# Optimization experiments

Measured on AMD Instinct MI355X. Metric: run time of the kernel, lower is better.

The kernel has to match this reference:

```python
import jax, jax.numpy as jnp
import numpy as np

TAU = 1.0
PAD_IDX = 0
EOS_IDX = 3
NEG = -10000000.0

B, T, H, E, V, BN = 256, 256, 1024, 512, 32000, 512


def setup_inputs() -> dict:
    key = jax.random.key(0)
    ks = jax.random.split(key, 30)
    s = lambda *sh: 0.02
    inp = {}
    inp['input_ids'] = jax.random.randint(ks[0], (B,), 0, V)
    inp['prediction'] = jax.random.normal(ks[1], (B, V), jnp.float32)
    inp['context'] = jax.random.normal(ks[2], (B, T, 2 * H), jnp.float32)
    inp['h0'] = jax.random.normal(ks[3], (2, B, H), jnp.float32)
    inp['mask'] = jax.random.randint(ks[4], (B, 8), 0, V)
    # parameters
    inp['embedding'] = jax.random.normal(ks[5], (V, E), jnp.float32) * 0.02
    inp['ge1_w'] = jax.random.normal(ks[6], (E, E), jnp.float32) * 0.02
    inp['ge1_b'] = jnp.zeros((E,), jnp.float32)
    inp['ge2_w'] = jax.random.normal(ks[7], (E, E), jnp.float32) * 0.02
    inp['ge2_b'] = jnp.zeros((E,), jnp.float32)
    inp['att_we'] = jax.random.normal(ks[8], (2 * H, H), jnp.float32) * 0.02
    inp['att_wd'] = jax.random.normal(ks[9], (H, H), jnp.float32) * 0.02
    inp['att_v'] = jax.random.normal(ks[10], (H,), jnp.float32) * 0.02
    in0 = 2 * H + E
    inp['wih0'] = jax.random.normal(ks[11], (3 * H, in0), jnp.float32) * 0.02
    inp['whh0'] = jax.random.normal(ks[12], (3 * H, H), jnp.float32) * 0.02
    inp['bih0'] = jnp.zeros((3 * H,), jnp.float32)
    inp['bhh0'] = jnp.zeros((3 * H,), jnp.float32)
    inp['wih1'] = jax.random.normal(ks[13], (3 * H, H), jnp.float32) * 0.02
    inp['whh1'] = jax.random.normal(ks[14], (3 * H, H), jnp.float32) * 0.02
    inp['bih1'] = jnp.zeros((3 * H,), jnp.float32)
    inp['bhh1'] = jnp.zeros((3 * H,), jnp.float32)
    inp['bn0_w'] = jax.random.normal(ks[15], (3 * H + E, BN), jnp.float32) * 0.02
    inp['bn0_b'] = jnp.zeros((BN,), jnp.float32)
    inp['bn1_w'] = jax.random.normal(ks[16], (BN, V), jnp.float32) * 0.02
    inp['bn1_b'] = jnp.zeros((V,), jnp.float32)
    return inp


def _gru_cell(x, h, wih, whh, bih, bhh):
    gi = x @ wih.T + bih  # [B, 3H]
    gh = h @ whh.T + bhh
    gi_r, gi_z, gi_n = jnp.split(gi, 3, axis=1)
    gh_r, gh_z, gh_n = jnp.split(gh, 3, axis=1)
    r = jax.nn.sigmoid(gi_r + gh_r)
    z = jax.nn.sigmoid(gi_z + gh_z)
    n = jnp.tanh(gi_n + r * gh_n)
    return (1.0 - z) * n + z * h


def _forward(input_ids, prediction, context, h0, mask, embedding,
             ge1_w, ge1_b, ge2_w, ge2_b, att_we, att_wd, att_v,
             wih0, whh0, bih0, bhh0, wih1, whh1, bih1, bhh1,
             bn0_w, bn0_b, bn1_w, bn1_b):
    embs = embedding[input_ids]  # [B, E]
    # global embedding gate
    probs = jax.nn.softmax(prediction / TAU, axis=1)  # [B, V]
    emb_avg = probs @ embedding  # [B, E]
    Hg = jax.nn.sigmoid(embs @ ge1_w + ge1_b + emb_avg @ ge2_w + ge2_b)
    embs = Hg * embs + (1.0 - Hg) * emb_avg
    # bahdanau attention with query = top-layer hidden
    q = h0[-1]  # [B, H]
    scores = jnp.tanh(context @ att_we + (q @ att_wd)[:, None, :]) @ att_v  # [B, T]
    attn = jax.nn.softmax(scores, axis=1)
    c_t = jnp.einsum('bt,btd->bd', attn, context)  # [B, 2H]
    rnn_in = jnp.concatenate([embs, c_t], axis=1)  # [B, E+2H]
    h1_0 = _gru_cell(rnn_in, h0[0], wih0, whh0, bih0, bhh0)
    h1_1 = _gru_cell(h1_0, h0[1], wih1, whh1, bih1, bhh1)
    output = h1_1
    h1 = jnp.stack([h1_0, h1_1])
    b0 = jnp.tanh(jnp.concatenate([output, c_t, embs], axis=1) @ bn0_w + bn0_b)
    pred = b0 @ bn1_w + bn1_b  # [B, V]
    # masked scatter: forbid already-generated tokens, but keep PAD/EOS columns
    pad_col = pred[:, PAD_IDX]
    eos_col = pred[:, EOS_IDX]
    rows = jnp.arange(pred.shape[0])
    pred = pred.at[rows[:, None], mask].set(NEG)
    pred = pred.at[:, PAD_IDX].set(pad_col)
    pred = pred.at[:, EOS_IDX].set(eos_col)
    return pred, h1, attn


def reference(input_ids, prediction, context, h0, mask, embedding,
              ge1_w, ge1_b, ge2_w, ge2_b, att_we, att_wd, att_v,
              wih0, whh0, bih0, bhh0, wih1, whh1, bih1, bhh1,
              bn0_w, bn0_b, bn1_w, bn1_b):
    return _forward(input_ids, prediction, context, h0, mask, embedding,
                    ge1_w, ge1_b, ge2_w, ge2_b, att_we, att_wd, att_v,
                    wih0, whh0, bih0, bhh0, wih1, whh1, bih1, bhh1,
                    bn0_w, bn0_b, bn1_w, bn1_b)
```

## Files before the change

### kernel.cpp

```cpp
#include <hip/hip_runtime.h>
#include <hip/hip_bf16.h>


typedef unsigned short u16;
typedef unsigned int u32;
typedef float f32x4 __attribute__((ext_vector_type(4)));
typedef u32 u32x4 __attribute__((ext_vector_type(4)));
typedef __bf16 bf16x8 __attribute__((ext_vector_type(8)));
typedef short s16x8 __attribute__((ext_vector_type(8)));

__device__ __forceinline__ u16 f2bf(float x) {
  u32 u = __float_as_uint(x);
  u += 0x7fffu + ((u >> 16) & 1u);
  return (u16)(u >> 16);
}
__device__ __forceinline__ u32 pack2(float a, float b) {
  return (u32)f2bf(a) | ((u32)f2bf(b) << 16);
}
__device__ __forceinline__ u32 cvt2(float a, float b) {
  union { __bf16 h[2]; u32 w; } u;
  u.h[0] = (__bf16)a; u.h[1] = (__bf16)b;
  return u.w;
}
__device__ __forceinline__ float bf2f(u16 v) {
  return __uint_as_float((u32)v << 16);
}
__device__ __forceinline__ f32x4 mfma_bf16(s16x8 a, s16x8 b, f32x4 c) {
  union { s16x8 s; bf16x8 b; } ua, ub;
  ua.s = a; ub.s = b;
  return __builtin_amdgcn_mfma_f32_16x16x32_bf16(ua.b, ub.b, c, 0, 0, 0);
}
__device__ __forceinline__ void gll16(const void* g, void* l) {
  __builtin_amdgcn_global_load_lds((__attribute__((address_space(1))) void*)g,
                                   (__attribute__((address_space(3))) void*)l,
                                   16, 0, 0);
}
__device__ __forceinline__ float sigf(float x) { return 1.0f / (1.0f + __expf(-x)); }

__global__ __launch_bounds__(256) void k_cvt8(const float* __restrict__ s,
                                              u16* __restrict__ d)
{
  size_t i = ((size_t)blockIdx.x * 256 + threadIdx.x) * 8;
  const size_t stride = (size_t)gridDim.x * 2048;
  for (; i < 134217728ull; i += stride) {
    float4 a = *(const float4*)(s + i);
    float4 b = *(const float4*)(s + i + 4);
    u32x4 w = {cvt2(a.x, a.y), cvt2(a.z, a.w), cvt2(b.x, b.y), cvt2(b.z, b.w)};
    *(u32x4*)(d + i) = w;
  }
}

__global__ __launch_bounds__(512, 4) void k_scores_bf(
    const u16* __restrict__ A, const u16* __restrict__ weT,
    const float* __restrict__ qd, const float* __restrict__ att_v,
    float* __restrict__ scores)
{
  __shared__ u16 As[3][4096];
  __shared__ u16 Bs[3][8192];

  const int tid = threadIdx.x;
  const int lane = tid & 63, wid = tid >> 6;
  const int l15 = lane & 15, lg = lane >> 4;
  const int wm = wid >> 2, wn = wid & 3;

  const int f = blockIdx.x;
  const int xcd = f & 7, slot = f >> 3;
  const int ntile = slot & 3;
  const int mtile = (slot >> 2) * 8 + xcd;
  const int n0 = ntile * 256;
  const int m0 = mtile * 128;
  const int b = mtile >> 1;

  const int sslot = ((lane & 3) ^ ((lane >> 3) & 3)) * 8;
  const size_t asrc = (size_t)(m0 + wid * 16 + (lane >> 2)) * 2048 + sslot;
  size_t bsrc[2];
#pragma unroll
  for (int i = 0; i < 2; ++i)
    bsrc[i] = (size_t)(n0 + (wid * 2 + i) * 16 + (lane >> 2)) * 2048 + sslot;

  const int rslot = (lg ^ ((l15 >> 1) & 3)) * 8;
  int aoff[4], boff[4];
#pragma unroll
  for (int mf = 0; mf < 4; ++mf) aoff[mf] = (wm * 64 + mf * 16 + l15) * 32 + rslot;
#pragma unroll
  for (int nf = 0; nf < 4; ++nf) boff[nf] = (wn * 64 + nf * 16 + l15) * 32 + rslot;

  f32x4 acc[4][4];
#pragma unroll
  for (int mf = 0; mf < 4; ++mf)
#pragma unroll
    for (int nf = 0; nf < 4; ++nf) acc[mf][nf] = (f32x4){0.f, 0.f, 0.f, 0.f};

  u16* As0 = &As[0][0];
  u16* Bs0 = &Bs[0][0];

  {
    gll16(A + asrc, As0 + wid * 512);
#pragma unroll
    for (int i = 0; i < 2; ++i)
      gll16(weT + bsrc[i], Bs0 + (wid * 2 + i) * 512);
    gll16(A + asrc + 32, As0 + 4096 + wid * 512);
#pragma unroll
    for (int i = 0; i < 2; ++i)
      gll16(weT + bsrc[i] + 32, Bs0 + 8192 + (wid * 2 + i) * 512);
  }

  int cur = 0, stg = 2;
  for (int kt = 0; kt < 64; ++kt) {
    if (kt < 63) asm volatile("s_waitcnt vmcnt(3)" ::: "memory");
    else         asm volatile("s_waitcnt vmcnt(0)" ::: "memory");
    __builtin_amdgcn_s_barrier();
    __builtin_amdgcn_sched_barrier(0);
    if (kt + 2 < 64) {
      gll16(A + asrc + (size_t)(kt + 2) * 32, As0 + stg * 4096 + wid * 512);
#pragma unroll
      for (int i = 0; i < 2; ++i)
        gll16(weT + bsrc[i] + (size_t)(kt + 2) * 32,
              Bs0 + stg * 8192 + (wid * 2 + i) * 512);
    }
    s16x8 af[4], bf[4];
#pragma unroll
    for (int mf = 0; mf < 4; ++mf)
      af[mf] = *(const s16x8*)(As0 + cur * 4096 + aoff[mf]);
#pragma unroll
    for (int nf = 0; nf < 4; ++nf)
      bf[nf] = *(const s16x8*)(Bs0 + cur * 8192 + boff[nf]);
    __builtin_amdgcn_s_setprio(1);
#pragma unroll
    for (int nf = 0; nf < 4; ++nf)
#pragma unroll
      for (int mf = 0; mf < 4; ++mf)
        acc[mf][nf] = mfma_bf16(af[mf], bf[nf], acc[mf][nf]);
    __builtin_amdgcn_s_setprio(0);
    cur = (cur == 2) ? 0 : cur + 1;
    stg = (stg == 2) ? 0 : stg + 1;
  }

  float rp[4][4] = {{0.f, 0.f, 0.f, 0.f}, {0.f, 0.f, 0.f, 0.f},
                    {0.f, 0.f, 0.f, 0.f}, {0.f, 0.f, 0.f, 0.f}};
#pragma unroll
  for (int nf = 0; nf < 4; ++nf) {
    int col = n0 + wn * 64 + nf * 16 + l15;
    float qv = qd[(size_t)b * 1024 + col];
    float vv = att_v[col];
#pragma unroll
    for (int mf = 0; mf < 4; ++mf)
#pragma unroll
      for (int e = 0; e < 4; ++e)
        rp[mf][e] += tanhf(acc[mf][nf][e] + qv) * vv;
  }
#pragma unroll
  for (int d = 1; d < 16; d <<= 1)
#pragma unroll
    for (int mf = 0; mf < 4; ++mf)
#pragma unroll
      for (int e = 0; e < 4; ++e)
        rp[mf][e] += __shfl_xor(rp[mf][e], d);
  if (l15 == 0) {
#pragma unroll
    for (int mf = 0; mf < 4; ++mf)
#pragma unroll
      for (int e = 0; e < 4; ++e)
        atomicAdd(&scores[(size_t)m0 + wm * 64 + mf * 16 + lg * 4 + e], rp[mf][e]);
  }
}

__global__ __launch_bounds__(256, 3) void k_scores(
    const float* __restrict__ ctx, const u16* __restrict__ weT,
    const float* __restrict__ qd, const float* __restrict__ att_v,
    float* __restrict__ scores)
{
  __shared__ u16 As[2][4096];
  __shared__ u16 Bs[2][4096];

  const int tid = threadIdx.x;
  const int lane = tid & 63, wid = tid >> 6;
  const int l15 = lane & 15, lg = lane >> 4;
  const int wm = wid >> 1, wn = wid & 1;
  const int n0 = blockIdx.x * 128;
  const int m0 = blockIdx.y * 128;
  const int b = blockIdx.y >> 1;

  const int r0 = tid >> 3, c4 = tid & 7;
  const float* actx = ctx + (size_t)(m0 + r0) * 2048 + c4 * 4;
  const int awoff = r0 * 32 + c4 * 4;

  size_t bsrc[2];
#pragma unroll
  for (int i = 0; i < 2; ++i)
    bsrc[i] = (size_t)(n0 + (wid * 2 + i) * 16 + (lane >> 2)) * 2048 + (size_t)(lane & 3) * 8;

  int aoff[4], boff[4];
#pragma unroll
  for (int mf = 0; mf < 4; ++mf) aoff[mf] = (wm * 64 + mf * 16 + l15) * 32 + lg * 8;
#pragma unroll
  for (int nf = 0; nf < 4; ++nf) boff[nf] = (wn * 64 + nf * 16 + l15) * 32 + lg * 8;

  f32x4 acc[4][4];
#pragma unroll
  for (int mf = 0; mf < 4; ++mf)
#pragma unroll
    for (int nf = 0; nf < 4; ++nf) acc[mf][nf] = (f32x4){0.f, 0.f, 0.f, 0.f};

  {
#pragma unroll
    for (int i = 0; i < 2; ++i)
      gll16(weT + bsrc[i], &Bs[0][(wid * 2 + i) * 512]);
#pragma unroll
    for (int j = 0; j < 4; ++j) {
      float4 av = *(const float4*)(actx + (size_t)(j * 32) * 2048);
      u32* w = (u32*)&As[0][awoff + j * 1024];
      w[0] = cvt2(av.x, av.y); w[1] = cvt2(av.z, av.w);
    }
  }
  __syncthreads();

  for (int kt = 0; kt < 64; ++kt) {
    const int cur = kt & 1, nxt = cur ^ 1;
    const bool pf = (kt < 63);
    float4 av[4];
    if (pf) {
#pragma unroll
      for (int i = 0; i < 2; ++i)
        gll16(weT + bsrc[i] + (size_t)(kt + 1) * 32, &Bs[nxt][(wid * 2 + i) * 512]);
#pragma unroll
      for (int j = 0; j < 4; ++j)
        av[j] = *(const float4*)(actx + (size_t)(j * 32) * 2048 + (kt + 1) * 32);
    }
    s16x8 af[4], bf[4];
#pragma unroll
    for (int mf = 0; mf < 4; ++mf) af[mf] = *(const s16x8*)(&As[cur][0] + aoff[mf]);
#pragma unroll
    for (int nf = 0; nf < 4; ++nf) bf[nf] = *(const s16x8*)(&Bs[cur][0] + boff[nf]);
#pragma unroll
    for (int nf = 0; nf < 4; ++nf)
#pragma unroll
      for (int mf = 0; mf < 4; ++mf)
        acc[mf][nf] = mfma_bf16(af[mf], bf[nf], acc[mf][nf]);
    if (pf) {
#pragma unroll
      for (int j = 0; j < 4; ++j) {
        u32* w = (u32*)&As[nxt][awoff + j * 1024];
        w[0] = cvt2(av[j].x, av[j].y); w[1] = cvt2(av[j].z, av[j].w);
      }
    }
    __syncthreads();
  }

  float rp[4][4] = {{0.f, 0.f, 0.f, 0.f}, {0.f, 0.f, 0.f, 0.f},
                    {0.f, 0.f, 0.f, 0.f}, {0.f, 0.f, 0.f, 0.f}};
#pragma unroll
  for (int nf = 0; nf < 4; ++nf) {
    int col = n0 + wn * 64 + nf * 16 + l15;
    float qv = qd[(size_t)b * 1024 + col];
    float vv = att_v[col];
#pragma unroll
    for (int mf = 0; mf < 4; ++mf)
#pragma unroll
      for (int e = 0; e < 4; ++e)
        rp[mf][e] += tanhf(acc[mf][nf][e] + qv) * vv;
  }
#pragma unroll
  for (int d = 1; d < 16; d <<= 1)
#pragma unroll
    for (int mf = 0; mf < 4; ++mf)
#pragma unroll
      for (int e = 0; e < 4; ++e)
        rp[mf][e] += __shfl_xor(rp[mf][e], d);
  if (l15 == 0) {
#pragma unroll
    for (int mf = 0; mf < 4; ++mf)
#pragma unroll
      for (int e = 0; e < 4; ++e)
        atomicAdd(&scores[(size_t)m0 + wm * 64 + mf * 16 + lg * 4 + e], rp[mf][e]);
  }
}

template <int MODE>
__global__ __launch_bounds__(256, 2) void k_gemm(
    const u16* __restrict__ A, const float* __restrict__ W,
    float* __restrict__ C, const float* __restrict__ bias,
    int N, int K, int ksteps_per, int tot_ksteps, int atomic_mode)
{
  __shared__ u16 As[2][8192];
  __shared__ u16 Bs[2][2048];
  const int tid = threadIdx.x, lane = tid & 63, wid = tid >> 6;
  const int l15 = lane & 15, lg = lane >> 4;
  const int m0 = blockIdx.x * 256;
  const int n0 = blockIdx.y * 64;
  const int kc0 = blockIdx.z * ksteps_per;
  int kcn = tot_ksteps - kc0;
  if (kcn > ksteps_per) kcn = ksteps_per;

  size_t asrc[4];
#pragma unroll
  for (int j = 0; j < 4; ++j)
    asrc[j] = (size_t)(m0 + wid * 64 + j * 16 + (lane >> 2)) * K + (size_t)(lane & 3) * 8;
  int aoff[4], boff[4];
#pragma unroll
  for (int mf = 0; mf < 4; ++mf) aoff[mf] = (wid * 64 + mf * 16 + l15) * 32 + lg * 8;
#pragma unroll
  for (int nf = 0; nf < 4; ++nf) boff[nf] = (nf * 16 + l15) * 32 + lg * 8;

  const int b_row = tid >> 2, b_c8 = tid & 3;
  const int b_kk = tid >> 3, b_c4 = tid & 7;

  f32x4 acc[4][4];
#pragma unroll
  for (int mf = 0; mf < 4; ++mf)
#pragma unroll
    for (int nf = 0; nf < 4; ++nf) acc[mf][nf] = (f32x4){0.f, 0.f, 0.f, 0.f};

  {
#pragma unroll
    for (int j = 0; j < 4; ++j)
      gll16(A + asrc[j] + (size_t)kc0 * 32, &As[0][wid * 2048 + j * 512]);
    if (MODE == 0) {
      const float* p = W + (size_t)(n0 + b_row) * K + (size_t)kc0 * 32 + b_c8 * 8;
      float4 v0 = *(const float4*)p, v1 = *(const float4*)(p + 4);
      u32* w = (u32*)&Bs[0][b_row * 32 + b_c8 * 8];
      w[0] = pack2(v0.x, v0.y); w[1] = pack2(v0.z, v0.w);
      w[2] = pack2(v1.x, v1.y); w[3] = pack2(v1.z, v1.w);
    } else {
      const float* p = W + (size_t)(kc0 * 32 + b_kk) * N + n0 + b_c4 * 4;
      float4 v0 = *(const float4*)p;
      float4 v1 = *(const float4*)(p + 32);
      int r0 = b_c4 * 4, r1 = 32 + b_c4 * 4;
      Bs[0][(r0 + 0) * 32 + b_kk] = f2bf(v0.x);
      Bs[0][(r0 + 1) * 32 + b_kk] = f2bf(v0.y);
      Bs[0][(r0 + 2) * 32 + b_kk] = f2bf(v0.z);
      Bs[0][(r0 + 3) * 32 + b_kk] = f2bf(v0.w);
      Bs[0][(r1 + 0) * 32 + b_kk] = f2bf(v1.x);
      Bs[0][(r1 + 1) * 32 + b_kk] = f2bf(v1.y);
      Bs[0][(r1 + 2) * 32 + b_kk] = f2bf(v1.z);
      Bs[0][(r1 + 3) * 32 + b_kk] = f2bf(v1.w);
    }
  }
  __syncthreads();

  for (int s = 0; s < kcn; ++s) {
    const int cur = s & 1, nxt = cur ^ 1;
    const bool pf = (s + 1 < kcn);
    const int ktn = kc0 + s + 1;
    float4 v0, v1;
    if (pf) {
#pragma unroll
      for (int j = 0; j < 4; ++j)
        gll16(A + asrc[j] + (size_t)ktn * 32, &As[nxt][wid * 2048 + j * 512]);
      if (MODE == 0) {
        const float* p = W + (size_t)(n0 + b_row) * K + (size_t)ktn * 32 + b_c8 * 8;
        v0 = *(const float4*)p; v1 = *(const float4*)(p + 4);
      } else {
        const float* p = W + (size_t)(ktn * 32 + b_kk) * N + n0 + b_c4 * 4;
        v0 = *(const float4*)p;
        v1 = *(const float4*)(p + 32);
      }
    }
    s16x8 af[4], bf[4];
#pragma unroll
    for (int mf = 0; mf < 4; ++mf) af[mf] = *(const s16x8*)(&As[cur][0] + aoff[mf]);
#pragma unroll
    for (int nf = 0; nf < 4; ++nf) bf[nf] = *(const s16x8*)(&Bs[cur][0] + boff[nf]);
#pragma unroll
    for (int nf = 0; nf < 4; ++nf)
#pragma unroll
      for (int mf = 0; mf < 4; ++mf)
        acc[mf][nf] = mfma_bf16(af[mf], bf[nf], acc[mf][nf]);
    if (pf) {
      if (MODE == 0) {
        u32* w = (u32*)&Bs[nxt][b_row * 32 + b_c8 * 8];
        w[0] = pack2(v0.x, v0.y); w[1] = pack2(v0.z, v0.w);
        w[2] = pack2(v1.x, v1.y); w[3] = pack2(v1.z, v1.w);
      } else {
        int r0 = b_c4 * 4, r1 = 32 + b_c4 * 4;
        Bs[nxt][(r0 + 0) * 32 + b_kk] = f2bf(v0.x);
        Bs[nxt][(r0 + 1) * 32 + b_kk] = f2bf(v0.y);
        Bs[nxt][(r0 + 2) * 32 + b_kk] = f2bf(v0.z);
        Bs[nxt][(r0 + 3) * 32 + b_kk] = f2bf(v0.w);
        Bs[nxt][(r1 + 0) * 32 + b_kk] = f2bf(v1.x);
        Bs[nxt][(r1 + 1) * 32 + b_kk] = f2bf(v1.y);
        Bs[nxt][(r1 + 2) * 32 + b_kk] = f2bf(v1.z);
        Bs[nxt][(r1 + 3) * 32 + b_kk] = f2bf(v1.w);
      }
    }
    __syncthreads();
  }

  const size_t Ns = (size_t)N;
#pragma unroll
  for (int mf = 0; mf < 4; ++mf)
#pragma unroll
    for (int nf = 0; nf < 4; ++nf) {
      int col = n0 + nf * 16 + l15;
#pragma unroll
      for (int e = 0; e < 4; ++e) {
        int row = m0 + wid * 64 + mf * 16 + lg * 4 + e;
        float v = acc[mf][nf][e];
        if (atomic_mode) atomicAdd(&C[row * Ns + col], v);
        else C[row * Ns + col] = v + (bias ? bias[col] : 0.0f);
      }
    }
}

__global__ __launch_bounds__(256) void k_prep(
    const float* __restrict__ we, u16* __restrict__ weT,
    const float* __restrict__ h0, u16* __restrict__ h0_bf,
    const int* __restrict__ ids, const float* __restrict__ emb,
    float* __restrict__ e0, u16* __restrict__ e0b)
{
  __shared__ float t[32][33];
  const int bid = blockIdx.x, tid = threadIdx.x;
  if (bid < 2048) {
    const int n0 = (bid & 31) * 32, k0 = (bid >> 5) * 32;
#pragma unroll
    for (int p = 0; p < 4; ++p) {
      int e = tid + p * 256, r = e >> 5, c = e & 31;
      t[r][c] = we[(size_t)(k0 + r) * 1024 + n0 + c];
    }
    __syncthreads();
#pragma unroll
    for (int p = 0; p < 4; ++p) {
      int e = tid + p * 256, n = e >> 5, k = e & 31;
      weT[(size_t)(n0 + n) * 2048 + k0 + k] = f2bf(t[k][n]);
    }
  } else if (bid < 4096) {
    int i = (bid - 2048) * 256 + tid;
    h0_bf[i] = f2bf(h0[i]);
  } else {
    int b = bid - 4096;
    int id = ids[b];
    for (int i = tid; i < 512; i += 256) {
      float v = emb[(size_t)id * 512 + i];
      e0[(size_t)b * 512 + i] = v;
      e0b[(size_t)b * 512 + i] = f2bf(v);
    }
  }
}

__global__ void k_cast(const float* __restrict__ s, u16* __restrict__ d, int n)
{
  int i = blockIdx.x * 256 + threadIdx.x;
  if (i < n) d[i] = f2bf(s[i]);
}

__global__ __launch_bounds__(1024) void k_softmax_pred(const float* __restrict__ pred,
                                                       u16* __restrict__ probs)
{
  __shared__ u16 xrow[32000];
  __shared__ float smM[16], smS[16];
  const int row = blockIdx.x, tid = threadIdx.x;
  const float* x = pred + (size_t)row * 32000;
  float m = -3.0e38f, s = 0.f;
  for (int i = tid; i < 32000; i += 1024) {
    u16 bv = f2bf(x[i]);
    xrow[i] = bv;
    float vr = bf2f(bv);
    if (vr > m) { s = s * __expf(m - vr) + 1.0f; m = vr; }
    else s += __expf(vr - m);
  }
#pragma unroll
  for (int d = 1; d < 64; d <<= 1) {
    float mo = __shfl_xor(m, d), so = __shfl_xor(s, d);
    float M = fmaxf(m, mo);
    s = s * __expf(m - M) + so * __expf(mo - M);
    m = M;
  }
  if ((tid & 63) == 0) { smM[tid >> 6] = m; smS[tid >> 6] = s; }
  __syncthreads();
  float M = -3.0e38f;
#pragma unroll
  for (int w = 0; w < 16; ++w) M = fmaxf(M, smM[w]);
  float S = 0.f;
#pragma unroll
  for (int w = 0; w < 16; ++w) S += smS[w] * __expf(smM[w] - M);
  float inv = 1.0f / S;
  for (int i = tid; i < 32000; i += 1024)
    probs[(size_t)row * 32000 + i] = f2bf(__expf(bf2f(xrow[i]) - M) * inv);
}

__global__ __launch_bounds__(256) void k_softmax_sc(const float* __restrict__ sc,
                                                    float* __restrict__ attn)
{
  __shared__ float sm[4];
  const int row = blockIdx.x, tid = threadIdx.x;
  float x = sc[(size_t)row * 256 + tid];
  float mx = x;
#pragma unroll
  for (int d = 1; d < 64; d <<= 1) mx = fmaxf(mx, __shfl_xor(mx, d));
  if ((tid & 63) == 0) sm[tid >> 6] = mx;
  __syncthreads();
  mx = fmaxf(fmaxf(sm[0], sm[1]), fmaxf(sm[2], sm[3]));
  float e = __expf(x - mx);
  float s = e;
#pragma unroll
  for (int d = 1; d < 64; d <<= 1) s += __shfl_xor(s, d);
  __syncthreads();
  if ((tid & 63) == 0) sm[tid >> 6] = s;
  __syncthreads();
  s = sm[0] + sm[1] + sm[2] + sm[3];
  attn[(size_t)row * 256 + tid] = e / s;
}

__global__ __launch_bounds__(256) void k_attn_ct(
    const float* __restrict__ sc, const u16* __restrict__ ctxb,
    float* __restrict__ attn, float* __restrict__ c_t)
{
  __shared__ float sm[4];
  __shared__ float att[256];
  const int b = blockIdx.y, tid = threadIdx.x;
  float x = sc[(size_t)b * 256 + tid];
  float mx = x;
#pragma unroll
  for (int d = 1; d < 64; d <<= 1) mx = fmaxf(mx, __shfl_xor(mx, d));
  if ((tid & 63) == 0) sm[tid >> 6] = mx;
  __syncthreads();
  mx = fmaxf(fmaxf(sm[0], sm[1]), fmaxf(sm[2], sm[3]));
  float e = __expf(x - mx);
  float s = e;
#pragma unroll
  for (int d = 1; d < 64; d <<= 1) s += __shfl_xor(s, d);
  __syncthreads();
  if ((tid & 63) == 0) sm[tid >> 6] = s;
  __syncthreads();
  s = sm[0] + sm[1] + sm[2] + sm[3];
  float a = e / s;
  att[tid] = a;
  if (blockIdx.x == 0) attn[(size_t)b * 256 + tid] = a;
  __syncthreads();

  const int d0 = blockIdx.x * 512 + tid * 2;
  const u16* cp = ctxb + (size_t)b * 524288 + d0;
  float a0 = 0.f, a1 = 0.f;
#pragma unroll 8
  for (int t = 0; t < 256; ++t) {
    float av = att[t];
    ushort2 v = *(const ushort2*)(cp + (size_t)t * 2048);
    a0 += av * bf2f(v.x); a1 += av * bf2f(v.y);
  }
  float2* o = (float2*)(c_t + (size_t)b * 2048 + d0);
  *o = (float2){a0, a1};
}

__global__ __launch_bounds__(256) void k_ct(const float* __restrict__ ctx,
                                            const float* __restrict__ attn,
                                            float* __restrict__ c_t)
{
  const int b = blockIdx.y;
  const int d0 = blockIdx.x * 512 + threadIdx.x * 2;
  const float2* cp = (const float2*)(ctx + (size_t)b * 524288 + d0);
  const float* ar = attn + (size_t)b * 256;
  float ax = 0.f, ay = 0.f;
#pragma unroll 4
  for (int t = 0; t < 256; ++t) {
    float a = ar[t];
    float2 v = cp[(size_t)t * 1024];
    ax += a * v.x; ay += a * v.y;
  }
  c_t[(size_t)b * 2048 + d0] = ax;
  c_t[(size_t)b * 2048 + d0 + 1] = ay;
}

__global__ void k_gate_cat(const float* __restrict__ gepre, const float* __restrict__ b1,
                           const float* __restrict__ b2, const float* __restrict__ e0,
                           const float* __restrict__ ea, float* __restrict__ embs,
                           const float* __restrict__ ct, u16* __restrict__ out)
{
  int i = blockIdx.x * 256 + threadIdx.x;
  int m = i / 2560, c = i - m * 2560;
  float v;
  if (c < 512) {
    int idx = m * 512 + c;
    float hg = sigf(gepre[idx] + b1[c] + b2[c]);
    v = hg * e0[idx] + (1.0f - hg) * ea[idx];
    embs[idx] = v;
  } else {
    v = ct[(size_t)m * 2048 + (c - 512)];
  }
  out[i] = f2bf(v);
}

__global__ void k_gru(const float* __restrict__ gi, const float* __restrict__ gh,
                      const float* __restrict__ bih, const float* __restrict__ bhh,
                      const float* __restrict__ hprev, float* __restrict__ hout,
                      u16* __restrict__ hout_bf)
{
  int i = blockIdx.x * 256 + threadIdx.x;
  int m = i >> 10, h = i & 1023;
  const float* gim = gi + (size_t)m * 3072;
  const float* ghm = gh + (size_t)m * 3072;
  float r = sigf(gim[h] + bih[h] + ghm[h] + bhh[h]);
  float z = sigf(gim[1024 + h] + bih[1024 + h] + ghm[1024 + h] + bhh[1024 + h]);
  float n = tanhf(gim[2048 + h] + bih[2048 + h] + r * (ghm[2048 + h] + bhh[2048 + h]));
  float hv = (1.0f - z) * n + z * hprev[i];
  hout[i] = hv;
  if (hout_bf) hout_bf[i] = f2bf(hv);
}

__global__ void k_cat_bn0(const float* __restrict__ h11, const float* __restrict__ ct,
                          const float* __restrict__ embs, u16* __restrict__ out)
{
  int i = blockIdx.x * 256 + threadIdx.x;
  int m = i / 3584, c = i - m * 3584;
  float v;
  if (c < 1024) v = h11[(size_t)m * 1024 + c];
  else if (c < 3072) v = ct[(size_t)m * 2048 + (c - 1024)];
  else v = embs[(size_t)m * 512 + (c - 3072)];
  out[i] = f2bf(v);
}

__global__ void k_bn0(const float* __restrict__ pre, const float* __restrict__ bias,
                      u16* __restrict__ b0b)
{
  int i = blockIdx.x * 256 + threadIdx.x;
  int nn = i & 511;
  b0b[i] = f2bf(tanhf(pre[i] + bias[nn]));
}

__global__ void k_mask(const int* __restrict__ mask, float* __restrict__ pred)
{
  int t = blockIdx.x * 256 + threadIdx.x;
  if (t >= 2048) return;
  int b = t >> 3;
  int col = mask[t];
  if (col != 0 && col != 3) pred[(size_t)b * 32000 + col] = -10000000.0f;
}

extern "C" void kernel_launch(void* const* d_in, const int* in_sizes, int n_in,
                              void* d_out, int out_size, void* d_ws, size_t ws_size,
                              hipStream_t stream)
{
  const int*   input_ids = (const int*)d_in[0];
  const float* prediction= (const float*)d_in[1];
  const float* context   = (const float*)d_in[2];
  const float* h0        = (const float*)d_in[3];
  const int*   maskp     = (const int*)d_in[4];
  const float* embedding = (const float*)d_in[5];
  const float* ge1_w = (const float*)d_in[6];
  const float* ge1_b = (const float*)d_in[7];
  const float* ge2_w = (const float*)d_in[8];
  const float* ge2_b = (const float*)d_in[9];
  const float* att_we = (const float*)d_in[10];
  const float* att_wd = (const float*)d_in[11];
  const float* att_v  = (const float*)d_in[12];
  const float* wih0 = (const float*)d_in[13];
  const float* whh0 = (const float*)d_in[14];
  const float* bih0 = (const float*)d_in[15];
  const float* bhh0 = (const float*)d_in[16];
  const float* wih1 = (const float*)d_in[17];
  const float* whh1 = (const float*)d_in[18];
  const float* bih1 = (const float*)d_in[19];
  const float* bhh1 = (const float*)d_in[20];
  const float* bn0_w = (const float*)d_in[21];
  const float* bn0_b = (const float*)d_in[22];
  const float* bn1_w = (const float*)d_in[23];
  const float* bn1_b = (const float*)d_in[24];

  float* out = (float*)d_out;
  float* out_pred = out;
  float* out_h1_0 = out + 8192000;
  float* out_h1_1 = out + 8454144;
  float* out_attn = out + 8716288;

  char* ws = (char*)d_ws;
  float* qd      = (float*)(ws + 0);
  float* emb_avg = (float*)(ws + 1048576);
  float* gepre   = (float*)(ws + 1572864);
  float* gi0     = (float*)(ws + 2097152);
  float* gh0     = (float*)(ws + 5242880);
  float* gi1     = (float*)(ws + 8388608);
  float* gh1     = (float*)(ws + 11534336);
  float* bn0pre  = (float*)(ws + 14680064);
  float* scores  = (float*)(ws + 15204352);
  const size_t MS_BYTES = 15466496;
  float* c_t     = (float*)(ws + 15466496);
  float* embs0   = (float*)(ws + 17563648);
  float* embs    = (float*)(ws + 18087936);
  u16* weT       = (u16*)(ws + 18612224);
  u16* h0_bf     = (u16*)(ws + 22806528);
  u16* embs0_bf  = (u16*)(ws + 23855104);
  u16* probs_bf  = (u16*)(ws + 24117248);
  u16* embavg_bf = (u16*)(ws + 40501248);
  u16* rnnin_bf  = (u16*)(ws + 40763392);
  u16* h1_0_bf   = (u16*)(ws + 42074112);
  u16* bn0in_bf  = (u16*)(ws + 42598400);
  u16* b0_bf     = (u16*)(ws + 44433408);
  u16* ctx_bf    = (u16*)(ws + 44695552);
  const bool big = ws_size >= 44695552ull + 268435456ull;

  (void)in_sizes; (void)n_in; (void)out_size;

  hipMemsetAsync(ws, 0, MS_BYTES, stream);

  if (big) k_cvt8<<<8192, 256, 0, stream>>>(context, ctx_bf);
  k_prep<<<4352, 256, 0, stream>>>(att_we, weT, h0, h0_bf, input_ids, embedding,
                                   embs0, embs0_bf);
  k_softmax_pred<<<256, 1024, 0, stream>>>(prediction, probs_bf);

  k_gemm<1><<<dim3(1, 16, 8), 256, 0, stream>>>(h0_bf + 262144, att_wd, qd, nullptr,
                                                1024, 1024, 4, 32, 1);
  if (big)
    k_scores_bf<<<2048, 512, 0, stream>>>(ctx_bf, weT, qd, att_v, scores);
  else
    k_scores<<<dim3(8, 512), 256, 0, stream>>>(context, weT, qd, att_v, scores);

  k_gemm<1><<<dim3(1, 8, 50), 256, 0, stream>>>(probs_bf, embedding, emb_avg, nullptr,
                                                512, 32000, 20, 1000, 1);
  k_cast<<<512, 256, 0, stream>>>(emb_avg, embavg_bf, 131072);
  k_gemm<1><<<dim3(1, 8, 4), 256, 0, stream>>>(embs0_bf, ge1_w, gepre, nullptr,
                                               512, 512, 4, 16, 1);
  k_gemm<1><<<dim3(1, 8, 4), 256, 0, stream>>>(embavg_bf, ge2_w, gepre, nullptr,
                                               512, 512, 4, 16, 1);

  if (big) {
    k_attn_ct<<<dim3(4, 256), 256, 0, stream>>>(scores, ctx_bf, out_attn, c_t);
  } else {
    k_softmax_sc<<<256, 256, 0, stream>>>(scores, out_attn);
    k_ct<<<dim3(4, 256), 256, 0, stream>>>(context, out_attn, c_t);
  }

  k_gate_cat<<<2560, 256, 0, stream>>>(gepre, ge1_b, ge2_b, embs0, emb_avg,
                                       embs, c_t, rnnin_bf);

  k_gemm<0><<<dim3(1, 48, 5), 256, 0, stream>>>(rnnin_bf, wih0, gi0, nullptr,
                                                3072, 2560, 16, 80, 1);
  k_gemm<0><<<dim3(1, 48, 4), 256, 0, stream>>>(h0_bf, whh0, gh0, nullptr,
                                                3072, 1024, 8, 32, 1);
  k_gru<<<1024, 256, 0, stream>>>(gi0, gh0, bih0, bhh0, h0, out_h1_0, h1_0_bf);
  k_gemm<0><<<dim3(1, 48, 4), 256, 0, stream>>>(h1_0_bf, wih1, gi1, nullptr,
                                                3072, 1024, 8, 32, 1);
  k_gemm<0><<<dim3(1, 48, 4), 256, 0, stream>>>(h0_bf + 262144, whh1, gh1, nullptr,
                                                3072, 1024, 8, 32, 1);
  k_gru<<<1024, 256, 0, stream>>>(gi1, gh1, bih1, bhh1, h0 + 262144, out_h1_1, nullptr);

  k_cat_bn0<<<3584, 256, 0, stream>>>(out_h1_1, c_t, embs, bn0in_bf);
  k_gemm<1><<<dim3(1, 8, 16), 256, 0, stream>>>(bn0in_bf, bn0_w, bn0pre, nullptr,
                                                512, 3584, 7, 112, 1);
  k_bn0<<<512, 256, 0, stream>>>(bn0pre, bn0_b, b0_bf);
  k_gemm<1><<<dim3(1, 500, 1), 256, 0, stream>>>(b0_bf, bn1_w, out_pred, bn1_b,
                                                 32000, 512, 16, 16, 0);
  k_mask<<<8, 256, 0, stream>>>(maskp, out_pred);
}
```

Before: 802.2 us.

## Drop bf16 context pre-conversion; convert fp32 context inline in scores GEMM

Removes the separate pass that converted the 512 MB fp32 context to bf16. The scores kernel now loads fp32 context directly and converts it to bf16 while staging into LDS, with a double buffer in place of the triple-buffered async load pipeline. The fused softmax and context kernel now reads fp32 context directly. This drops a full read and write of the context tensor. In exchange the scores main loop does register-staged loads and conversion with a barrier every iteration, and the c_t reduction reads twice as many bytes.

```diff
diff --git a/kernel.cpp b/kernel.cpp
--- a/kernel.cpp
+++ b/kernel.cpp
@@ -37,26 +37,13 @@
 }
 __device__ __forceinline__ float sigf(float x) { return 1.0f / (1.0f + __expf(-x)); }
 
-__global__ __launch_bounds__(256) void k_cvt8(const float* __restrict__ s,
-                                              u16* __restrict__ d)
-{
-  size_t i = ((size_t)blockIdx.x * 256 + threadIdx.x) * 8;
-  const size_t stride = (size_t)gridDim.x * 2048;
-  for (; i < 134217728ull; i += stride) {
-    float4 a = *(const float4*)(s + i);
-    float4 b = *(const float4*)(s + i + 4);
-    u32x4 w = {cvt2(a.x, a.y), cvt2(a.z, a.w), cvt2(b.x, b.y), cvt2(b.z, b.w)};
-    *(u32x4*)(d + i) = w;
-  }
-}
-
-__global__ __launch_bounds__(512, 4) void k_scores_bf(
-    const u16* __restrict__ A, const u16* __restrict__ weT,
+__global__ __launch_bounds__(512, 4) void k_scores_f32(
+    const float* __restrict__ ctx, const u16* __restrict__ weT,
     const float* __restrict__ qd, const float* __restrict__ att_v,
     float* __restrict__ scores)
 {
-  __shared__ u16 As[3][4096];
-  __shared__ u16 Bs[3][8192];
+  __shared__ u16 As[2][4096];
+  __shared__ u16 Bs[2][8192];
 
   const int tid = threadIdx.x;
   const int lane = tid & 63, wid = tid >> 6;
@@ -71,8 +58,11 @@
   const int m0 = mtile * 128;
   const int b = mtile >> 1;
 
+  const int arow = tid >> 2, ac8 = (tid & 3) * 8;
+  const float* actx = ctx + (size_t)(m0 + arow) * 2048 + ac8;
+  const int awoff = arow * 32 + ac8;
+
   const int sslot = ((lane & 3) ^ ((lane >> 3) & 3)) * 8;
-  const size_t asrc = (size_t)(m0 + wid * 16 + (lane >> 2)) * 2048 + sslot;
   size_t bsrc[2];
 #pragma unroll
   for (int i = 0; i < 2; ++i)
@@ -81,7 +71,7 @@
   const int rslot = (lg ^ ((l15 >> 1) & 3)) * 8;
   int aoff[4], boff[4];
 #pragma unroll
-  for (int mf = 0; mf < 4; ++mf) aoff[mf] = (wm * 64 + mf * 16 + l15) * 32 + rslot;
+  for (int mf = 0; mf < 4; ++mf) aoff[mf] = (wm * 64 + mf * 16 + l15) * 32 + lg * 8;
 #pragma unroll
   for (int nf = 0; nf < 4; ++nf) boff[nf] = (wn * 64 + nf * 16 + l15) * 32 + rslot;
 
@@ -91,40 +81,33 @@
 #pragma unroll
     for (int nf = 0; nf < 4; ++nf) acc[mf][nf] = (f32x4){0.f, 0.f, 0.f, 0.f};
 
-  u16* As0 = &As[0][0];
-  u16* Bs0 = &Bs[0][0];
-
   {
-    gll16(A + asrc, As0 + wid * 512);
 #pragma unroll
     for (int i = 0; i < 2; ++i)
-      gll16(weT + bsrc[i], Bs0 + (wid * 2 + i) * 512);
-    gll16(A + asrc + 32, As0 + 4096 + wid * 512);
-#pragma unroll
-    for (int i = 0; i < 2; ++i)
-      gll16(weT + bsrc[i] + 32, Bs0 + 8192 + (wid * 2 + i) * 512);
-  }
-
-  int cur = 0, stg = 2;
+      gll16(weT + bsrc[i], &Bs[0][(wid * 2 + i) * 512]);
+    float4 a0 = *(const float4*)(actx);
+    float4 a1 = *(const float4*)(actx + 4);
+    u32x4 w = {cvt2(a0.x, a0.y), cvt2(a0.z, a0.w), cvt2(a1.x, a1.y), cvt2(a1.z, a1.w)};
+    *(u32x4*)&As[0][awoff] = w;
+  }
+  __syncthreads();
+
   for (int kt = 0; kt < 64; ++kt) {
-    if (kt < 63) asm volatile("s_waitcnt vmcnt(3)" ::: "memory");
-    else         asm volatile("s_waitcnt vmcnt(0)" ::: "memory");
-    __builtin_amdgcn_s_barrier();
-    __builtin_amdgcn_sched_barrier(0);
-    if (kt + 2 < 64) {
-      gll16(A + asrc + (size_t)(kt + 2) * 32, As0 + stg * 4096 + wid * 512);
+    const int cur = kt & 1, nxt = cur ^ 1;
+    const bool pf = (kt < 63);
+    float4 a0, a1;
+    if (pf) {
 #pragma unroll
       for (int i = 0; i < 2; ++i)
-        gll16(weT + bsrc[i] + (size_t)(kt + 2) * 32,
-              Bs0 + stg * 8192 + (wid * 2 + i) * 512);
+        gll16(weT + bsrc[i] + (size_t)(kt + 1) * 32, &Bs[nxt][(wid * 2 + i) * 512]);
+      a0 = *(const float4*)(actx + (size_t)(kt + 1) * 32);
+      a1 = *(const float4*)(actx + (size_t)(kt + 1) * 32 + 4);
     }
     s16x8 af[4], bf[4];
 #pragma unroll
-    for (int mf = 0; mf < 4; ++mf)
-      af[mf] = *(const s16x8*)(As0 + cur * 4096 + aoff[mf]);
-#pragma unroll
-    for (int nf = 0; nf < 4; ++nf)
-      bf[nf] = *(const s16x8*)(Bs0 + cur * 8192 + boff[nf]);
+    for (int mf = 0; mf < 4; ++mf) af[mf] = *(const s16x8*)(&As[cur][0] + aoff[mf]);
+#pragma unroll
+    for (int nf = 0; nf < 4; ++nf) bf[nf] = *(const s16x8*)(&Bs[cur][0] + boff[nf]);
     __builtin_amdgcn_s_setprio(1);
 #pragma unroll
     for (int nf = 0; nf < 4; ++nf)
@@ -132,117 +115,9 @@
       for (int mf = 0; mf < 4; ++mf)
         acc[mf][nf] = mfma_bf16(af[mf], bf[nf], acc[mf][nf]);
     __builtin_amdgcn_s_setprio(0);
-    cur = (cur == 2) ? 0 : cur + 1;
-    stg = (stg == 2) ? 0 : stg + 1;
-  }
-
-  float rp[4][4] = {{0.f, 0.f, 0.f, 0.f}, {0.f, 0.f, 0.f, 0.f},
-                    {0.f, 0.f, 0.f, 0.f}, {0.f, 0.f, 0.f, 0.f}};
-#pragma unroll
-  for (int nf = 0; nf < 4; ++nf) {
-    int col = n0 + wn * 64 + nf * 16 + l15;
-    float qv = qd[(size_t)b * 1024 + col];
-    float vv = att_v[col];
-#pragma unroll
-    for (int mf = 0; mf < 4; ++mf)
-#pragma unroll
-      for (int e = 0; e < 4; ++e)
-        rp[mf][e] += tanhf(acc[mf][nf][e] + qv) * vv;
-  }
-#pragma unroll
-  for (int d = 1; d < 16; d <<= 1)
-#pragma unroll
-    for (int mf = 0; mf < 4; ++mf)
-#pragma unroll
-      for (int e = 0; e < 4; ++e)
-        rp[mf][e] += __shfl_xor(rp[mf][e], d);
-  if (l15 == 0) {
-#pragma unroll
-    for (int mf = 0; mf < 4; ++mf)
-#pragma unroll
-      for (int e = 0; e < 4; ++e)
-        atomicAdd(&scores[(size_t)m0 + wm * 64 + mf * 16 + lg * 4 + e], rp[mf][e]);
-  }
-}
-
-__global__ __launch_bounds__(256, 3) void k_scores(
-    const float* __restrict__ ctx, const u16* __restrict__ weT,
-    const float* __restrict__ qd, const float* __restrict__ att_v,
-    float* __restrict__ scores)
-{
-  __shared__ u16 As[2][4096];
-  __shared__ u16 Bs[2][4096];
-
-  const int tid = threadIdx.x;
-  const int lane = tid & 63, wid = tid >> 6;
-  const int l15 = lane & 15, lg = lane >> 4;
-  const int wm = wid >> 1, wn = wid & 1;
-  const int n0 = blockIdx.x * 128;
-  const int m0 = blockIdx.y * 128;
-  const int b = blockIdx.y >> 1;
-
-  const int r0 = tid >> 3, c4 = tid & 7;
-  const float* actx = ctx + (size_t)(m0 + r0) * 2048 + c4 * 4;
-  const int awoff = r0 * 32 + c4 * 4;
-
-  size_t bsrc[2];
-#pragma unroll
-  for (int i = 0; i < 2; ++i)
-    bsrc[i] = (size_t)(n0 + (wid * 2 + i) * 16 + (lane >> 2)) * 2048 + (size_t)(lane & 3) * 8;
-
-  int aoff[4], boff[4];
-#pragma unroll
-  for (int mf = 0; mf < 4; ++mf) aoff[mf] = (wm * 64 + mf * 16 + l15) * 32 + lg * 8;
-#pragma unroll
-  for (int nf = 0; nf < 4; ++nf) boff[nf] = (wn * 64 + nf * 16 + l15) * 32 + lg * 8;
-
-  f32x4 acc[4][4];
-#pragma unroll
-  for (int mf = 0; mf < 4; ++mf)
-#pragma unroll
-    for (int nf = 0; nf < 4; ++nf) acc[mf][nf] = (f32x4){0.f, 0.f, 0.f, 0.f};
-
-  {
-#pragma unroll
-    for (int i = 0; i < 2; ++i)
-      gll16(weT + bsrc[i], &Bs[0][(wid * 2 + i) * 512]);
-#pragma unroll
-    for (int j = 0; j < 4; ++j) {
-      float4 av = *(const float4*)(actx + (size_t)(j * 32) * 2048);
-      u32* w = (u32*)&As[0][awoff + j * 1024];
-      w[0] = cvt2(av.x, av.y); w[1] = cvt2(av.z, av.w);
-    }
-  }
-  __syncthreads();
-
-  for (int kt = 0; kt < 64; ++kt) {
-    const int cur = kt & 1, nxt = cur ^ 1;
-    const bool pf = (kt < 63);
-    float4 av[4];
     if (pf) {
-#pragma unroll
-      for (int i = 0; i < 2; ++i)
-        gll16(weT + bsrc[i] + (size_t)(kt + 1) * 32, &Bs[nxt][(wid * 2 + i) * 512]);
-#pragma unroll
-      for (int j = 0; j < 4; ++j)
-        av[j] = *(const float4*)(actx + (size_t)(j * 32) * 2048 + (kt + 1) * 32);
-    }
-    s16x8 af[4], bf[4];
-#pragma unroll
-    for (int mf = 0; mf < 4; ++mf) af[mf] = *(const s16x8*)(&As[cur][0] + aoff[mf]);
-#pragma unroll
-    for (int nf = 0; nf < 4; ++nf) bf[nf] = *(const s16x8*)(&Bs[cur][0] + boff[nf]);
-#pragma unroll
-    for (int nf = 0; nf < 4; ++nf)
-#pragma unroll
-      for (int mf = 0; mf < 4; ++mf)
-        acc[mf][nf] = mfma_bf16(af[mf], bf[nf], acc[mf][nf]);
-    if (pf) {
-#pragma unroll
-      for (int j = 0; j < 4; ++j) {
-        u32* w = (u32*)&As[nxt][awoff + j * 1024];
-        w[0] = cvt2(av[j].x, av[j].y); w[1] = cvt2(av[j].z, av[j].w);
-      }
+      u32x4 w = {cvt2(a0.x, a0.y), cvt2(a0.z, a0.w), cvt2(a1.x, a1.y), cvt2(a1.z, a1.w)};
+      *(u32x4*)&As[nxt][awoff] = w;
     }
     __syncthreads();
   }
@@ -478,31 +353,8 @@
     probs[(size_t)row * 32000 + i] = f2bf(__expf(bf2f(xrow[i]) - M) * inv);
 }
 
-__global__ __launch_bounds__(256) void k_softmax_sc(const float* __restrict__ sc,
-                                                    float* __restrict__ attn)
-{
-  __shared__ float sm[4];
-  const int row = blockIdx.x, tid = threadIdx.x;
-  float x = sc[(size_t)row * 256 + tid];
-  float mx = x;
-#pragma unroll
-  for (int d = 1; d < 64; d <<= 1) mx = fmaxf(mx, __shfl_xor(mx, d));
-  if ((tid & 63) == 0) sm[tid >> 6] = mx;
-  __syncthreads();
-  mx = fmaxf(fmaxf(sm[0], sm[1]), fmaxf(sm[2], sm[3]));
-  float e = __expf(x - mx);
-  float s = e;
-#pragma unroll
-  for (int d = 1; d < 64; d <<= 1) s += __shfl_xor(s, d);
-  __syncthreads();
-  if ((tid & 63) == 0) sm[tid >> 6] = s;
-  __syncthreads();
-  s = sm[0] + sm[1] + sm[2] + sm[3];
-  attn[(size_t)row * 256 + tid] = e / s;
-}
-
 __global__ __launch_bounds__(256) void k_attn_ct(
-    const float* __restrict__ sc, const u16* __restrict__ ctxb,
+    const float* __restrict__ sc, const float* __restrict__ ctx,
     float* __restrict__ attn, float* __restrict__ c_t)
 {
   __shared__ float sm[4];
@@ -529,35 +381,16 @@
   __syncthreads();
 
   const int d0 = blockIdx.x * 512 + tid * 2;
-  const u16* cp = ctxb + (size_t)b * 524288 + d0;
+  const float2* cp = (const float2*)(ctx + (size_t)b * 524288 + d0);
   float a0 = 0.f, a1 = 0.f;
 #pragma unroll 8
   for (int t = 0; t < 256; ++t) {
     float av = att[t];
-    ushort2 v = *(const ushort2*)(cp + (size_t)t * 2048);
-    a0 += av * bf2f(v.x); a1 += av * bf2f(v.y);
+    float2 v = cp[(size_t)t * 1024];
+    a0 += av * v.x; a1 += av * v.y;
   }
   float2* o = (float2*)(c_t + (size_t)b * 2048 + d0);
   *o = (float2){a0, a1};
-}
-
-__global__ __launch_bounds__(256) void k_ct(const float* __restrict__ ctx,
-                                            const float* __restrict__ attn,
-                                            float* __restrict__ c_t)
-{
-  const int b = blockIdx.y;
-  const int d0 = blockIdx.x * 512 + threadIdx.x * 2;
-  const float2* cp = (const float2*)(ctx + (size_t)b * 524288 + d0);
-  const float* ar = attn + (size_t)b * 256;
-  float ax = 0.f, ay = 0.f;
-#pragma unroll 4
-  for (int t = 0; t < 256; ++t) {
-    float a = ar[t];
-    float2 v = cp[(size_t)t * 1024];
-    ax += a * v.x; ay += a * v.y;
-  }
-  c_t[(size_t)b * 2048 + d0] = ax;
-  c_t[(size_t)b * 2048 + d0 + 1] = ay;
 }
 
 __global__ void k_gate_cat(const float* __restrict__ gepre, const float* __restrict__ b1,
@@ -684,24 +517,18 @@
   u16* h1_0_bf   = (u16*)(ws + 42074112);
   u16* bn0in_bf  = (u16*)(ws + 42598400);
   u16* b0_bf     = (u16*)(ws + 44433408);
-  u16* ctx_bf    = (u16*)(ws + 44695552);
-  const bool big = ws_size >= 44695552ull + 268435456ull;
-
-  (void)in_sizes; (void)n_in; (void)out_size;
+
+  (void)in_sizes; (void)n_in; (void)out_size; (void)ws_size;
 
   hipMemsetAsync(ws, 0, MS_BYTES, stream);
 
-  if (big) k_cvt8<<<8192, 256, 0, stream>>>(context, ctx_bf);
   k_prep<<<4352, 256, 0, stream>>>(att_we, weT, h0, h0_bf, input_ids, embedding,
                                    embs0, embs0_bf);
   k_softmax_pred<<<256, 1024, 0, stream>>>(prediction, probs_bf);
 
   k_gemm<1><<<dim3(1, 16, 8), 256, 0, stream>>>(h0_bf + 262144, att_wd, qd, nullptr,
                                                 1024, 1024, 4, 32, 1);
-  if (big)
-    k_scores_bf<<<2048, 512, 0, stream>>>(ctx_bf, weT, qd, att_v, scores);
-  else
-    k_scores<<<dim3(8, 512), 256, 0, stream>>>(context, weT, qd, att_v, scores);
+  k_scores_f32<<<2048, 512, 0, stream>>>(context, weT, qd, att_v, scores);
 
   k_gemm<1><<<dim3(1, 8, 50), 256, 0, stream>>>(probs_bf, embedding, emb_avg, nullptr,
                                                 512, 32000, 20, 1000, 1);
@@ -711,12 +538,7 @@
   k_gemm<1><<<dim3(1, 8, 4), 256, 0, stream>>>(embavg_bf, ge2_w, gepre, nullptr,
                                                512, 512, 4, 16, 1);
 
-  if (big) {
-    k_attn_ct<<<dim3(4, 256), 256, 0, stream>>>(scores, ctx_bf, out_attn, c_t);
-  } else {
-    k_softmax_sc<<<256, 256, 0, stream>>>(scores, out_attn);
-    k_ct<<<dim3(4, 256), 256, 0, stream>>>(context, out_attn, c_t);
-  }
+  k_attn_ct<<<dim3(4, 256), 256, 0, stream>>>(scores, context, out_attn, c_t);
 
   k_gate_cat<<<2560, 256, 0, stream>>>(gepre, ge1_b, ge2_b, embs0, emb_avg,
                                        embs, c_t, rnnin_bf);
```

Result: no change. 786.9 us (-1.9%).
